# Kernel optimization log

Hardware: AMD Instinct MI355X
Metric: run time of the kernel (lower is better)

Reference implementation:

```python
import jax, jax.numpy as jnp
import numpy as np

B, N, NREL = 8, 512, 4096
IN_DIM, REL_DIM = 64, 32
NF_PART, NF_REL, NF_EFF, OUT_DIM = 128, 256, 128, 64


def _lin(key, fan_in, fan_out):
    kw, kb = jax.random.split(key)
    s = 1.0 / np.sqrt(fan_in)
    w = jax.random.uniform(kw, (fan_in, fan_out), jnp.float32, -s, s)
    b = jax.random.uniform(kb, (fan_out,), jnp.float32, -s, s)
    return w, b


def setup_inputs() -> dict:
    key = jax.random.key(0)
    ks = jax.random.split(key, 16)
    state = jax.random.normal(ks[0], (B, N, IN_DIM), jnp.float32)
    # one-hot receiver / sender incidence matrices [B, N, NREL]
    recv = jax.random.randint(ks[1], (B, NREL), 0, N)
    send = jax.random.randint(ks[2], (B, NREL), 0, N)
    Rr = jnp.transpose(jax.nn.one_hot(recv, N, dtype=jnp.float32), (0, 2, 1))
    Rs = jnp.transpose(jax.nn.one_hot(send, N, dtype=jnp.float32), (0, 2, 1))
    Ra = jax.random.normal(ks[3], (B, NREL, REL_DIM), jnp.float32)

    pe0_w, pe0_b = _lin(ks[4], IN_DIM, NF_PART)
    pe1_w, pe1_b = _lin(ks[5], NF_PART, NF_PART)
    pe2_w, pe2_b = _lin(ks[6], NF_PART, NF_EFF)
    re_in = 2 * IN_DIM + REL_DIM
    re0_w, re0_b = _lin(ks[7], re_in, NF_REL)
    re1_w, re1_b = _lin(ks[8], NF_REL, NF_REL)
    re2_w, re2_b = _lin(ks[9], NF_REL, NF_REL)
    rp_w, rp_b = _lin(ks[10], NF_REL + 2 * NF_EFF, NF_EFF)   # relation propagator
    pp_w, pp_b = _lin(ks[11], 2 * NF_EFF, NF_EFF)            # particle propagator
    pr0_w, pr0_b = _lin(ks[12], NF_EFF, NF_EFF)
    pr1_w, pr1_b = _lin(ks[13], NF_EFF, OUT_DIM)

    return dict(state=state, Rr=Rr, Rs=Rs, Ra=Ra,
                pe0_w=pe0_w, pe0_b=pe0_b, pe1_w=pe1_w, pe1_b=pe1_b,
                pe2_w=pe2_w, pe2_b=pe2_b,
                re0_w=re0_w, re0_b=re0_b, re1_w=re1_w, re1_b=re1_b,
                re2_w=re2_w, re2_b=re2_b,
                rp_w=rp_w, rp_b=rp_b, pp_w=pp_w, pp_b=pp_b,
                pr0_w=pr0_w, pr0_b=pr0_b, pr1_w=pr1_w, pr1_b=pr1_b,
                pstep=3)


def _mlp3(x, w0, b0, w1, b1, w2, b2):
    x = jax.nn.relu(x @ w0 + b0)
    x = jax.nn.relu(x @ w1 + b1)
    return jax.nn.relu(x @ w2 + b2)


def reference(state, Rr, Rs, Ra,
              pe0_w, pe0_b, pe1_w, pe1_b, pe2_w, pe2_b,
              re0_w, re0_b, re1_w, re1_b, re2_w, re2_b,
              rp_w, rp_b, pp_w, pp_b,
              pr0_w, pr0_b, pr1_w, pr1_b, pstep):
    Rrp = jnp.transpose(Rr, (0, 2, 1))  # [B, NREL, N]
    Rsp = jnp.transpose(Rs, (0, 2, 1))
    state_r = Rrp @ state               # [B, NREL, IN_DIM]
    state_s = Rsp @ state

    particle_encode = _mlp3(state, pe0_w, pe0_b, pe1_w, pe1_b, pe2_w, pe2_b)
    relation_encode = _mlp3(jnp.concatenate([state_r, state_s, Ra], axis=2),
                            re0_w, re0_b, re1_w, re1_b, re2_w, re2_b)

    particle_effect = jnp.zeros((state.shape[0], state.shape[1], NF_EFF),
                                dtype=state.dtype)
    for _ in range(pstep):
        effect_r = Rrp @ particle_effect           # gather to relations
        effect_s = Rsp @ particle_effect
        relation_effect = jax.nn.relu(
            jnp.concatenate([relation_encode, effect_r, effect_s], axis=2)
            @ rp_w + rp_b)
        effect_agg = Rr @ relation_effect          # scatter to particles
        particle_effect = jax.nn.relu(
            jnp.concatenate([particle_encode, effect_agg], axis=2)
            @ pp_w + pp_b)

    h = jax.nn.relu(particle_effect @ pr0_w + pr0_b)
    return h @ pr1_w + pr1_b                       # [B, N, OUT_DIM]
```

## Files before the change

### kernel.cpp

```cpp
#include <hip/hip_runtime.h>
#include <hip/hip_bf16.h>

#define BC    8
#define NC    512
#define NRELC 4096
#define MAXDEG 64

typedef unsigned short u16;
typedef __attribute__((ext_vector_type(2))) float  f32x2;
typedef __attribute__((ext_vector_type(4))) float  f32x4;
typedef __attribute__((ext_vector_type(8))) __bf16 bf16x8;
typedef __attribute__((ext_vector_type(8))) short  s16x8;
typedef __attribute__((ext_vector_type(2))) u16    u16x2;
typedef __attribute__((ext_vector_type(4))) u16    u16x4;
typedef __attribute__((ext_vector_type(4))) int    i32x4;

__device__ __forceinline__ u16 f2b(float f) {
  union { float f; unsigned u; } v; v.f = f;
  unsigned u = v.u;
  return (u16)((u + 0x7fffu + ((u >> 16) & 1u)) >> 16);
}
__device__ __forceinline__ float b2f(u16 h) {
  union { unsigned u; float f; } v; v.u = ((unsigned)h) << 16; return v.f;
}

template<int KBLK>
__device__ __forceinline__ int toff(int row, int k) {
  return (row >> 4) * (KBLK * 256) + ((k >> 3) << 8) + ((row & 15) << 4) + ((k & 7) << 1);
}

__global__ __launch_bounds__(1024, 8) void onehot_matvec_v2(
    const float* __restrict__ Rr, const float* __restrict__ Rs,
    int* __restrict__ recv, int* __restrict__ send) {
  int blk = blockIdx.x;
  int tens = blk >> 8;
  int b = (blk >> 5) & 7;
  int rt = blk & 31;
  const float* srcf = (tens ? Rs : Rr) + (long)b * NC * NRELC + rt * 128;
  int* dst = (tens ? send : recv) + b * NRELC + rt * 128;
  int tid = threadIdx.x;
  int ng = tid >> 5;
  int col = tid & 31;
  const f32x4* cp = (const f32x4*)srcf + col;
  f32x4 acc = (f32x4){0.f, 0.f, 0.f, 0.f};
#pragma unroll
  for (int i = 0; i < 16; ++i) {
    int n = ng * 16 + i;
    f32x4 x = cp[(long)n * (NRELC / 4)];
    float w = (float)n;
    acc[0] = fmaf(x[0], w, acc[0]);
    acc[1] = fmaf(x[1], w, acc[1]);
    acc[2] = fmaf(x[2], w, acc[2]);
    acc[3] = fmaf(x[3], w, acc[3]);
  }
  __shared__ f32x4 red[1024];
  red[tid] = acc;
  __syncthreads();
  if (tid < 32) {
    f32x4 s = red[tid];
#pragma unroll
    for (int g = 1; g < 32; ++g) {
      f32x4 t = red[g * 32 + tid];
      s[0] += t[0]; s[1] += t[1]; s[2] += t[2]; s[3] += t[3];
    }
    i32x4 o;
    o[0] = (int)s[0]; o[1] = (int)s[1]; o[2] = (int)s[2]; o[3] = (int)s[3];
    *(i32x4*)&dst[tid * 4] = o;
  }
}

struct WT13 {
  const float* src[13];
  u16* dst[13];
  int K[13], N[13];
  int cum[14];
};

__global__ void wtrans_v2(WT13 wt) {
  int idx = blockIdx.x * 256 + threadIdx.x;
  if (idx >= wt.cum[13]) return;
  int w = 0;
  while (idx >= wt.cum[w + 1]) ++w;
  int j = idx - wt.cum[w];
  int N = wt.N[w], K = wt.K[w];
  int k = j / N, n = j - k * N;
  wt.dst[w][n * K + k] = f2b(wt.src[w][j]);
}

template<int MT, int NT, bool AF32>
__device__ __forceinline__ void tile_gemm(const void* __restrict__ Ap, long rowBase,
                                          const u16* __restrict__ Wt, int n0,
                                          int K, int rl, int kg, f32x4 acc[MT][NT]) {
#pragma unroll
  for (int mt = 0; mt < MT; ++mt)
#pragma unroll
    for (int t = 0; t < NT; ++t) acc[mt][t] = (f32x4){0.f, 0.f, 0.f, 0.f};

  for (int k0 = 0; k0 < K; k0 += 32) {
    int kk = k0 + kg * 8;
    bf16x8 af[MT];
#pragma unroll
    for (int mt = 0; mt < MT; ++mt) {
      long row = rowBase + mt * 16 + rl;
      if (AF32) {
        const float* ap = (const float*)Ap + row * K + kk;
        f32x4 lo = *(const f32x4*)ap;
        f32x4 hi = *(const f32x4*)(ap + 4);
        s16x8 s;
        s[0] = (short)f2b(lo[0]); s[1] = (short)f2b(lo[1]);
        s[2] = (short)f2b(lo[2]); s[3] = (short)f2b(lo[3]);
        s[4] = (short)f2b(hi[0]); s[5] = (short)f2b(hi[1]);
        s[6] = (short)f2b(hi[2]); s[7] = (short)f2b(hi[3]);
        af[mt] = __builtin_bit_cast(bf16x8, s);
      } else {
        af[mt] = *reinterpret_cast<const bf16x8*>((const u16*)Ap + row * K + kk);
      }
    }
#pragma unroll
    for (int t = 0; t < NT; ++t) {
      bf16x8 bf = *reinterpret_cast<const bf16x8*>(Wt + (size_t)(n0 + t * 16 + rl) * K + kk);
#pragma unroll
      for (int mt = 0; mt < MT; ++mt)
        acc[mt][t] = __builtin_amdgcn_mfma_f32_16x16x32_bf16(af[mt], bf, acc[mt][t], 0, 0, 0);
    }
  }
}

__global__ __launch_bounds__(256) void csr_partenc_v2(
    const int* __restrict__ recv, int* __restrict__ deg, int* __restrict__ lists,
    const float* __restrict__ state,
    const u16* __restrict__ pe0t, const float* __restrict__ pe0_b,
    const u16* __restrict__ pe1t, const float* __restrict__ pe1_b,
    const u16* __restrict__ pe2t, const float* __restrict__ pe2_b,
    const u16* __restrict__ pp0t, const float* __restrict__ pp_b,
    float* __restrict__ pbase) {
  __shared__ char t0[4096];
  __shared__ char t1[4096];
  int wid = threadIdx.x >> 6, lane = threadIdx.x & 63;
  if (blockIdx.x < 1024) {
    int bn = blockIdx.x * 4 + wid;
    int b = bn >> 9, n = bn & 511;
    const int* rv = recv + (long)b * NRELC;
    int base = 0;
    for (int c = 0; c < 64; ++c) {
      int r = c * 64 + lane;
      bool ok = (rv[r] == n);
      unsigned long long m = __ballot(ok);
      if (ok) {
        int rank = __popcll(m & ((1ull << lane) - 1ull));
        lists[(long)bn * MAXDEG + base + rank] = r;
      }
      base += (int)__popcll(m);
    }
    if (lane == 0) deg[bn] = base;
    return;
  }
  int rl = lane & 15, kg = lane >> 4;
  long rowBase = (blockIdx.x - 1024) * 16;

  f32x4 acc[1][2];
  tile_gemm<1, 2, true>(state, rowBase, pe0t, wid * 32, 64, rl, kg, acc);
#pragma unroll
  for (int t = 0; t < 2; ++t) {
    int gc = wid * 32 + t * 16 + rl;
    float bv = pe0_b[gc];
#pragma unroll
    for (int r = 0; r < 4; ++r)
      *(u16*)&t0[toff<16>(kg * 4 + r, gc)] = f2b(fmaxf(acc[0][t][r] + bv, 0.f));
  }
  __syncthreads();

  f32x4 a2[2];
  a2[0] = (f32x4){0.f, 0.f, 0.f, 0.f};
  a2[1] = (f32x4){0.f, 0.f, 0.f, 0.f};
#pragma unroll
  for (int ki = 0; ki < 4; ++ki) {
    int kk = ki * 32 + kg * 8;
    bf16x8 af = *(const bf16x8*)&t0[toff<16>(rl, kk)];
#pragma unroll
    for (int t = 0; t < 2; ++t) {
      bf16x8 bf = *(const bf16x8*)(pe1t + (size_t)(wid * 32 + t * 16 + rl) * 128 + kk);
      a2[t] = __builtin_amdgcn_mfma_f32_16x16x32_bf16(af, bf, a2[t], 0, 0, 0);
    }
  }
#pragma unroll
  for (int t = 0; t < 2; ++t) {
    int gc = wid * 32 + t * 16 + rl;
    float bv = pe1_b[gc];
#pragma unroll
    for (int r = 0; r < 4; ++r)
      *(u16*)&t1[toff<16>(kg * 4 + r, gc)] = f2b(fmaxf(a2[t][r] + bv, 0.f));
  }
  __syncthreads();

  a2[0] = (f32x4){0.f, 0.f, 0.f, 0.f};
  a2[1] = (f32x4){0.f, 0.f, 0.f, 0.f};
#pragma unroll
  for (int ki = 0; ki < 4; ++ki) {
    int kk = ki * 32 + kg * 8;
    bf16x8 af = *(const bf16x8*)&t1[toff<16>(rl, kk)];
#pragma unroll
    for (int t = 0; t < 2; ++t) {
      bf16x8 bf = *(const bf16x8*)(pe2t + (size_t)(wid * 32 + t * 16 + rl) * 128 + kk);
      a2[t] = __builtin_amdgcn_mfma_f32_16x16x32_bf16(af, bf, a2[t], 0, 0, 0);
    }
  }
#pragma unroll
  for (int t = 0; t < 2; ++t) {
    int gc = wid * 32 + t * 16 + rl;
    float bv = pe2_b[gc];
#pragma unroll
    for (int r = 0; r < 4; ++r)
      *(u16*)&t0[toff<16>(kg * 4 + r, gc)] = f2b(fmaxf(a2[t][r] + bv, 0.f));
  }
  __syncthreads();

  a2[0] = (f32x4){0.f, 0.f, 0.f, 0.f};
  a2[1] = (f32x4){0.f, 0.f, 0.f, 0.f};
#pragma unroll
  for (int ki = 0; ki < 4; ++ki) {
    int kk = ki * 32 + kg * 8;
    bf16x8 af = *(const bf16x8*)&t0[toff<16>(rl, kk)];
#pragma unroll
    for (int t = 0; t < 2; ++t) {
      bf16x8 bf = *(const bf16x8*)(pp0t + (size_t)(wid * 32 + t * 16 + rl) * 128 + kk);
      a2[t] = __builtin_amdgcn_mfma_f32_16x16x32_bf16(af, bf, a2[t], 0, 0, 0);
    }
  }
#pragma unroll
  for (int t = 0; t < 2; ++t) {
    int gc = wid * 32 + t * 16 + rl;
    float bv = pp_b[gc];
#pragma unroll
    for (int r = 0; r < 4; ++r) {
      long gr = rowBase + kg * 4 + r;
      pbase[gr * 128 + gc] = a2[t][r] + bv;
    }
  }
}

template<int KD, int NTt>
__device__ __forceinline__ void lds_layer_v4(const char* bufIn, const u16* __restrict__ Wt,
                                             int n0, int rl, int kg, f32x4 acc[4][NTt]) {
  constexpr int KI = KD / 32;
  bf16x8 bw[NTt][KI];
#pragma unroll
  for (int t = 0; t < NTt; ++t)
#pragma unroll
    for (int ki = 0; ki < KI; ++ki)
      bw[t][ki] = *(const bf16x8*)(Wt + (size_t)(n0 + t * 16 + rl) * KD + ki * 32 + kg * 8);
#pragma unroll
  for (int mt = 0; mt < 4; ++mt)
#pragma unroll
    for (int t = 0; t < NTt; ++t) acc[mt][t] = (f32x4){0.f, 0.f, 0.f, 0.f};
#pragma unroll
  for (int ki = 0; ki < KI; ++ki) {
    int kk = ki * 32 + kg * 8;
    bf16x8 af[4];
#pragma unroll
    for (int mt = 0; mt < 4; ++mt)
      af[mt] = *(const bf16x8*)&bufIn[toff<32>(mt * 16 + rl, kk)];
#pragma unroll
    for (int t = 0; t < NTt; ++t)
#pragma unroll
      for (int mt = 0; mt < 4; ++mt)
        acc[mt][t] = __builtin_amdgcn_mfma_f32_16x16x32_bf16(af[mt], bw[t][ki], acc[mt][t], 0, 0, 0);
  }
}

template<int NTt>
__device__ __forceinline__ void lds_store_v4(char* bufOut, const float* __restrict__ bias,
                                             int n0, int rl, int kg, f32x4 acc[4][NTt]) {
#pragma unroll
  for (int mt = 0; mt < 4; ++mt)
#pragma unroll
    for (int t = 0; t < NTt; ++t) {
      int gc = n0 + t * 16 + rl;
      float bv = bias[gc];
#pragma unroll
      for (int r = 0; r < 4; ++r) {
        int row = mt * 16 + kg * 4 + r;
        *(u16*)&bufOut[toff<32>(row, gc)] = f2b(fmaxf(acc[mt][t][r] + bv, 0.f));
      }
    }
}

__global__ __launch_bounds__(512, 3) void relenc_fused_v5(
    const float* __restrict__ state, const float* __restrict__ Ra,
    const int* __restrict__ recv, const int* __restrict__ send,
    const u16* __restrict__ re0t, const float* __restrict__ re0_b,
    const u16* __restrict__ re1t, const float* __restrict__ re1_b,
    const u16* __restrict__ re2t, const float* __restrict__ re2_b,
    const u16* __restrict__ rp0t, const float* __restrict__ rp_b,
    u16* __restrict__ rbase16) {
  __shared__ char bufA[32768];
  __shared__ char bufB[32768];
  int tid = threadIdx.x;
  int m0 = blockIdx.x * 64;

  for (int c = tid; c < 64 * 40; c += 512) {
    int row = c / 40;
    int c4 = (c - row * 40) * 4;
    int grow = m0 + row;
    int b = grow >> 12;
    f32x4 v;
    if (c4 < 64)       v = *(const f32x4*)&state[((long)(b * NC + recv[grow])) * 64 + c4];
    else if (c4 < 128) v = *(const f32x4*)&state[((long)(b * NC + send[grow])) * 64 + (c4 - 64)];
    else               v = *(const f32x4*)&Ra[(long)grow * 32 + (c4 - 128)];
    u16x4 o;
    o[0] = f2b(v[0]); o[1] = f2b(v[1]); o[2] = f2b(v[2]); o[3] = f2b(v[3]);
    *(u16x4*)&bufA[toff<32>(row, c4)] = o;
  }
  __syncthreads();

  int wid = tid >> 6, lane = tid & 63;
  int rl = lane & 15, kg = lane >> 4;

  f32x4 acc[4][2];
  lds_layer_v4<160, 2>(bufA, re0t, wid * 32, rl, kg, acc);
  lds_store_v4<2>(bufB, re0_b, wid * 32, rl, kg, acc);
  __syncthreads();
  lds_layer_v4<256, 2>(bufB, re1t, wid * 32, rl, kg, acc);
  lds_store_v4<2>(bufA, re1_b, wid * 32, rl, kg, acc);
  __syncthreads();
  lds_layer_v4<256, 2>(bufA, re2t, wid * 32, rl, kg, acc);
  lds_store_v4<2>(bufB, re2_b, wid * 32, rl, kg, acc);
  __syncthreads();
  f32x4 acc2[4][1];
  lds_layer_v4<256, 1>(bufB, rp0t, wid * 16, rl, kg, acc2);
#pragma unroll
  for (int mt = 0; mt < 4; ++mt) {
    int gc = wid * 16 + rl;
    float bv = rp_b[gc];
#pragma unroll
    for (int r = 0; r < 4; ++r) {
      long gr = m0 + mt * 16 + kg * 4 + r;
      rbase16[gr * 128 + gc] = f2b(acc2[mt][0][r] + bv);
    }
  }
}

__global__ __launch_bounds__(512, 4) void relstep_v5(
    const u16* __restrict__ peff, const u16* __restrict__ rp1t,
    const u16* __restrict__ rp2t, const u16* __restrict__ rbase16,
    const int* __restrict__ recv, const int* __restrict__ send,
    u16* __restrict__ tmp16) {
  __shared__ char ebuf0[16384];
  __shared__ char ebuf1[16384];
  int tid = threadIdx.x;
  int m0 = blockIdx.x * 64;

  for (int c = tid; c < 2048; c += 512) {
    int s = c >> 10, rem = c & 1023, row = rem >> 4, ch = rem & 15;
    int gr = m0 + row;
    int b = gr >> 12;
    int idx = s ? send[gr] : recv[gr];
    bf16x8 v = *(const bf16x8*)&peff[((long)(b * NC + idx)) * 128 + ch * 8];
    char* dst = s ? ebuf1 : ebuf0;
    *(bf16x8*)&dst[toff<16>(row, ch * 8)] = v;
  }
  __syncthreads();

  int wid = tid >> 6, lane = tid & 63;
  int rl = lane & 15, kg = lane >> 4;
  int wm = wid >> 2, wn = wid & 3;
  int n0 = wn * 32;

  bf16x8 b1[2][4], b2[2][4];
#pragma unroll
  for (int t = 0; t < 2; ++t)
#pragma unroll
    for (int ki = 0; ki < 4; ++ki) {
      b1[t][ki] = *(const bf16x8*)(rp1t + (size_t)(n0 + t * 16 + rl) * 128 + ki * 32 + kg * 8);
      b2[t][ki] = *(const bf16x8*)(rp2t + (size_t)(n0 + t * 16 + rl) * 128 + ki * 32 + kg * 8);
    }

  f32x4 acc[2][2];
#pragma unroll
  for (int mt = 0; mt < 2; ++mt)
#pragma unroll
    for (int t = 0; t < 2; ++t) acc[mt][t] = (f32x4){0.f, 0.f, 0.f, 0.f};

#pragma unroll
  for (int ki = 0; ki < 4; ++ki) {
    int kk = ki * 32 + kg * 8;
    bf16x8 e0[2], e1[2];
#pragma unroll
    for (int mt = 0; mt < 2; ++mt) {
      int row = wm * 32 + mt * 16 + rl;
      e0[mt] = *(const bf16x8*)&ebuf0[toff<16>(row, kk)];
      e1[mt] = *(const bf16x8*)&ebuf1[toff<16>(row, kk)];
    }
#pragma unroll
    for (int t = 0; t < 2; ++t)
#pragma unroll
      for (int mt = 0; mt < 2; ++mt)
        acc[mt][t] = __builtin_amdgcn_mfma_f32_16x16x32_bf16(e0[mt], b1[t][ki], acc[mt][t], 0, 0, 0);
#pragma unroll
    for (int t = 0; t < 2; ++t)
#pragma unroll
      for (int mt = 0; mt < 2; ++mt)
        acc[mt][t] = __builtin_amdgcn_mfma_f32_16x16x32_bf16(e1[mt], b2[t][ki], acc[mt][t], 0, 0, 0);
  }

#pragma unroll
  for (int mt = 0; mt < 2; ++mt) {
#pragma unroll
    for (int r = 0; r < 4; ++r) {
      long gr = m0 + wm * 32 + mt * 16 + kg * 4 + r;
      const u16* rb = &rbase16[gr * 128];
      u16* dst = &tmp16[gr * 128];
#pragma unroll
      for (int t = 0; t < 2; ++t) {
        int gc = n0 + t * 16 + rl;
        dst[gc] = f2b(fmaxf(acc[mt][t][r] + b2f(rb[gc]), 0.f));
      }
    }
  }
}

template<bool RELU>
__global__ __launch_bounds__(256) void segreduce_b16(
    const u16* __restrict__ src, const int* __restrict__ deg,
    const int* __restrict__ lists, u16* __restrict__ agg16) {
  int wid = threadIdx.x >> 6, lane = threadIdx.x & 63;
  int p = blockIdx.x * 4 + wid;
  int b = p >> 9;
  int c = lane * 2;
  int d = deg[p];
  const int* lp = &lists[(long)p * MAXDEG];
  f32x2 acc = (f32x2){0.f, 0.f};
  for (int k = 0; k < d; ++k) {
    long row = ((long)b * NRELC + lp[k]) * 128;
    u16x2 h = *(const u16x2*)&src[row + c];
    float v0 = b2f(h[0]), v1 = b2f(h[1]);
    if (RELU) { v0 = fmaxf(v0, 0.f); v1 = fmaxf(v1, 0.f); }
    acc[0] += v0; acc[1] += v1;
  }
  u16x2 o;
  o[0] = f2b(acc[0]); o[1] = f2b(acc[1]);
  *(u16x2*)&agg16[(long)p * 128 + c] = o;
}

__global__ __launch_bounds__(256) void ppgemm_v2(
    const u16* __restrict__ agg16, const u16* __restrict__ pp1t,
    const float* __restrict__ pbase, u16* __restrict__ peff) {
  int wid = threadIdx.x >> 6, lane = threadIdx.x & 63;
  int rl = lane & 15, kg = lane >> 4;
  long rowBase = blockIdx.x * 16;
  f32x4 acc[1][2];
  tile_gemm<1, 2, false>(agg16, rowBase, pp1t, wid * 32, 128, rl, kg, acc);
#pragma unroll
  for (int t = 0; t < 2; ++t) {
    int gc = wid * 32 + t * 16 + rl;
#pragma unroll
    for (int r = 0; r < 4; ++r) {
      long gr = rowBase + kg * 4 + r;
      float v = acc[0][t][r] + pbase[gr * 128 + gc];
      peff[gr * 128 + gc] = f2b(fmaxf(v, 0.f));
    }
  }
}

__global__ __launch_bounds__(256) void ppdec_kernel(
    const u16* __restrict__ agg16, const u16* __restrict__ pp1t,
    const float* __restrict__ pbase,
    const u16* __restrict__ pr0t, const float* __restrict__ pr0_b,
    const u16* __restrict__ pr1t, const float* __restrict__ pr1_b,
    float* __restrict__ out) {
  __shared__ char t0[4096];
  __shared__ char t1[4096];
  int wid = threadIdx.x >> 6, lane = threadIdx.x & 63;
  int rl = lane & 15, kg = lane >> 4;
  long rowBase = blockIdx.x * 16;

  f32x4 acc[1][2];
  tile_gemm<1, 2, false>(agg16, rowBase, pp1t, wid * 32, 128, rl, kg, acc);
#pragma unroll
  for (int t = 0; t < 2; ++t) {
    int gc = wid * 32 + t * 16 + rl;
#pragma unroll
    for (int r = 0; r < 4; ++r) {
      int row = kg * 4 + r;
      float v = acc[0][t][r] + pbase[(rowBase + row) * 128 + gc];
      *(u16*)&t0[toff<16>(row, gc)] = f2b(fmaxf(v, 0.f));
    }
  }
  __syncthreads();

  f32x4 a2[2];
  a2[0] = (f32x4){0.f, 0.f, 0.f, 0.f};
  a2[1] = (f32x4){0.f, 0.f, 0.f, 0.f};
#pragma unroll
  for (int ki = 0; ki < 4; ++ki) {
    int kk = ki * 32 + kg * 8;
    bf16x8 af = *(const bf16x8*)&t0[toff<16>(rl, kk)];
#pragma unroll
    for (int t = 0; t < 2; ++t) {
      bf16x8 bf = *(const bf16x8*)(pr0t + (size_t)(wid * 32 + t * 16 + rl) * 128 + kk);
      a2[t] = __builtin_amdgcn_mfma_f32_16x16x32_bf16(af, bf, a2[t], 0, 0, 0);
    }
  }
#pragma unroll
  for (int t = 0; t < 2; ++t) {
    int gc = wid * 32 + t * 16 + rl;
    float bv = pr0_b[gc];
#pragma unroll
    for (int r = 0; r < 4; ++r) {
      int row = kg * 4 + r;
      *(u16*)&t1[toff<16>(row, gc)] = f2b(fmaxf(a2[t][r] + bv, 0.f));
    }
  }
  __syncthreads();

  if (wid < 4) {
    f32x4 a3 = (f32x4){0.f, 0.f, 0.f, 0.f};
#pragma unroll
    for (int ki = 0; ki < 4; ++ki) {
      int kk = ki * 32 + kg * 8;
      bf16x8 af = *(const bf16x8*)&t1[toff<16>(rl, kk)];
      bf16x8 bf = *(const bf16x8*)(pr1t + (size_t)(wid * 16 + rl) * 128 + kk);
      a3 = __builtin_amdgcn_mfma_f32_16x16x32_bf16(af, bf, a3, 0, 0, 0);
    }
    int gc = wid * 16 + rl;
    float bv = pr1_b[gc];
#pragma unroll
    for (int r = 0; r < 4; ++r) {
      long gr = rowBase + kg * 4 + r;
      out[gr * 64 + gc] = a3[r] + bv;
    }
  }
}

extern "C" void kernel_launch(void* const* d_in, const int* in_sizes, int n_in,
                              void* d_out, int out_size, void* d_ws, size_t ws_size,
                              hipStream_t stream) {
  const float* state = (const float*)d_in[0];
  const float* Rr    = (const float*)d_in[1];
  const float* Rs    = (const float*)d_in[2];
  const float* Ra    = (const float*)d_in[3];
  const float* pe0_w = (const float*)d_in[4];  const float* pe0_b = (const float*)d_in[5];
  const float* pe1_w = (const float*)d_in[6];  const float* pe1_b = (const float*)d_in[7];
  const float* pe2_w = (const float*)d_in[8];  const float* pe2_b = (const float*)d_in[9];
  const float* re0_w = (const float*)d_in[10]; const float* re0_b = (const float*)d_in[11];
  const float* re1_w = (const float*)d_in[12]; const float* re1_b = (const float*)d_in[13];
  const float* re2_w = (const float*)d_in[14]; const float* re2_b = (const float*)d_in[15];
  const float* rp_w  = (const float*)d_in[16]; const float* rp_b  = (const float*)d_in[17];
  const float* pp_w  = (const float*)d_in[18]; const float* pp_b  = (const float*)d_in[19];
  const float* pr0_w = (const float*)d_in[20]; const float* pr0_b = (const float*)d_in[21];
  const float* pr1_w = (const float*)d_in[22]; const float* pr1_b = (const float*)d_in[23];

  char* base = (char*)d_ws; size_t off = 0;
  auto alloc = [&](size_t b) -> void* {
    void* p = base + off; off = (off + b + 255) & ~(size_t)255; return p;
  };

  int* recv  = (int*)alloc(4L * BC * NRELC);
  int* send  = (int*)alloc(4L * BC * NRELC);
  int* deg   = (int*)alloc(4L * BC * NC);
  int* lists = (int*)alloc(4L * BC * NC * MAXDEG);
  u16* pe0t = (u16*)alloc(2L * 128 * 64);
  u16* pe1t = (u16*)alloc(2L * 128 * 128);
  u16* pe2t = (u16*)alloc(2L * 128 * 128);
  u16* re0t = (u16*)alloc(2L * 256 * 160);
  u16* re1t = (u16*)alloc(2L * 256 * 256);
  u16* re2t = (u16*)alloc(2L * 256 * 256);
  u16* rp0t = (u16*)alloc(2L * 128 * 256);
  u16* rp1t = (u16*)alloc(2L * 128 * 128);
  u16* rp2t = (u16*)alloc(2L * 128 * 128);
  u16* pp0t = (u16*)alloc(2L * 128 * 128);
  u16* pp1t = (u16*)alloc(2L * 128 * 128);
  u16* pr0t = (u16*)alloc(2L * 128 * 128);
  u16* pr1t = (u16*)alloc(2L * 64 * 128);
  u16* tmp16   = (u16*)alloc(2L * 32768 * 128);
  u16* rbase16 = (u16*)alloc(2L * 32768 * 128);
  float* pbase = (float*)alloc(4L * 4096 * 128);
  u16* agg16 = (u16*)alloc(2L * 4096 * 128);
  u16* peff = (u16*)alloc(2L * 4096 * 128);
  (void)ws_size; (void)in_sizes; (void)n_in; (void)out_size;

  struct WSpec { const float* src; u16* dst; int K, N; };
  const WSpec specs[13] = {
      {pe0_w,            pe0t, 64, 128},
      {pe1_w,            pe1t, 128, 128},
      {pe2_w,            pe2t, 128, 128},
      {re0_w,            re0t, 160, 256},
      {re1_w,            re1t, 256, 256},
      {re2_w,            re2t, 256, 256},
      {rp_w,             rp0t, 256, 128},
      {rp_w + 256 * 128, rp1t, 128, 128},
      {rp_w + 384 * 128, rp2t, 128, 128},
      {pp_w,             pp0t, 128, 128},
      {pp_w + 128 * 128, pp1t, 128, 128},
      {pr0_w,            pr0t, 128, 128},
      {pr1_w,            pr1t, 128, 64},
  };
  WT13 wt;
  int cum = 0;
  for (int i = 0; i < 13; ++i) {
    wt.src[i] = specs[i].src; wt.dst[i] = specs[i].dst;
    wt.K[i] = specs[i].K; wt.N[i] = specs[i].N;
    wt.cum[i] = cum; cum += specs[i].K * specs[i].N;
  }
  wt.cum[13] = cum;

  onehot_matvec_v2<<<512, 1024, 0, stream>>>(Rr, Rs, recv, send);
  wtrans_v2<<<(cum + 255) / 256, 256, 0, stream>>>(wt);

  csr_partenc_v2<<<1280, 256, 0, stream>>>(recv, deg, lists, state,
                                           pe0t, pe0_b, pe1t, pe1_b, pe2t, pe2_b,
                                           pp0t, pp_b, pbase);
  relenc_fused_v5<<<512, 512, 0, stream>>>(state, Ra, recv, send,
                                           re0t, re0_b, re1t, re1_b, re2t, re2_b,
                                           rp0t, rp_b, rbase16);

  segreduce_b16<true><<<1024, 256, 0, stream>>>(rbase16, deg, lists, agg16);
  ppgemm_v2<<<256, 256, 0, stream>>>(agg16, pp1t, pbase, peff);
  for (int s = 1; s < 3; ++s) {
    relstep_v5<<<512, 512, 0, stream>>>(peff, rp1t, rp2t, rbase16, recv, send, tmp16);
    segreduce_b16<false><<<1024, 256, 0, stream>>>(tmp16, deg, lists, agg16);
    if (s == 2) break;
    ppgemm_v2<<<256, 256, 0, stream>>>(agg16, pp1t, pbase, peff);
  }

  ppdec_kernel<<<256, 256, 0, stream>>>(agg16, pp1t, pbase,
                                        pr0t, pr0_b, pr1t, pr1_b, (float*)d_out);
}
```

Baseline: 159.2 us.

## Fuse segment reduction with particle-propagator GEMM and decoder into one kernel

Merges the per-particle segment-sum over incident relations with the following particle-propagator GEMM, and in the last step also with the two decoder layers, into one 1024-thread kernel. Each block reduces 16 particles (one per wave) into shared memory, then four waves run the MFMA GEMM directly from LDS. This drops the agg16 intermediate buffer and three kernel launches. In exchange, 12 of the 16 waves sit idle during the GEMM phase and each block is large.

```diff
diff --git a/kernel.cpp b/kernel.cpp
--- a/kernel.cpp
+++ b/kernel.cpp
@@ -419,106 +419,120 @@
   }
 }
 
-template<bool RELU>
-__global__ __launch_bounds__(256) void segreduce_b16(
+template<bool SRELU, bool FINAL>
+__global__ __launch_bounds__(1024) void segpp_v3(
     const u16* __restrict__ src, const int* __restrict__ deg,
-    const int* __restrict__ lists, u16* __restrict__ agg16) {
-  int wid = threadIdx.x >> 6, lane = threadIdx.x & 63;
-  int p = blockIdx.x * 4 + wid;
-  int b = p >> 9;
-  int c = lane * 2;
-  int d = deg[p];
-  const int* lp = &lists[(long)p * MAXDEG];
-  f32x2 acc = (f32x2){0.f, 0.f};
-  for (int k = 0; k < d; ++k) {
-    long row = ((long)b * NRELC + lp[k]) * 128;
-    u16x2 h = *(const u16x2*)&src[row + c];
-    float v0 = b2f(h[0]), v1 = b2f(h[1]);
-    if (RELU) { v0 = fmaxf(v0, 0.f); v1 = fmaxf(v1, 0.f); }
-    acc[0] += v0; acc[1] += v1;
-  }
-  u16x2 o;
-  o[0] = f2b(acc[0]); o[1] = f2b(acc[1]);
-  *(u16x2*)&agg16[(long)p * 128 + c] = o;
-}
-
-__global__ __launch_bounds__(256) void ppgemm_v2(
-    const u16* __restrict__ agg16, const u16* __restrict__ pp1t,
-    const float* __restrict__ pbase, u16* __restrict__ peff) {
-  int wid = threadIdx.x >> 6, lane = threadIdx.x & 63;
-  int rl = lane & 15, kg = lane >> 4;
-  long rowBase = blockIdx.x * 16;
-  f32x4 acc[1][2];
-  tile_gemm<1, 2, false>(agg16, rowBase, pp1t, wid * 32, 128, rl, kg, acc);
-#pragma unroll
-  for (int t = 0; t < 2; ++t) {
-    int gc = wid * 32 + t * 16 + rl;
-#pragma unroll
-    for (int r = 0; r < 4; ++r) {
-      long gr = rowBase + kg * 4 + r;
-      float v = acc[0][t][r] + pbase[gr * 128 + gc];
-      peff[gr * 128 + gc] = f2b(fmaxf(v, 0.f));
-    }
-  }
-}
-
-__global__ __launch_bounds__(256) void ppdec_kernel(
-    const u16* __restrict__ agg16, const u16* __restrict__ pp1t,
-    const float* __restrict__ pbase,
+    const int* __restrict__ lists, const u16* __restrict__ pp1t,
+    const float* __restrict__ pbase, u16* __restrict__ peff,
     const u16* __restrict__ pr0t, const float* __restrict__ pr0_b,
     const u16* __restrict__ pr1t, const float* __restrict__ pr1_b,
     float* __restrict__ out) {
   __shared__ char t0[4096];
   __shared__ char t1[4096];
-  int wid = threadIdx.x >> 6, lane = threadIdx.x & 63;
+  int tid = threadIdx.x, wid = tid >> 6, lane = tid & 63;
+  long p0 = (long)blockIdx.x * 16;
+
+  {
+    int p = (int)p0 + wid;
+    int b = p >> 9;
+    int c = lane * 2;
+    int d = deg[p];
+    const int* lp = &lists[(long)p * MAXDEG];
+    f32x2 a = (f32x2){0.f, 0.f};
+    for (int k = 0; k < d; ++k) {
+      long row = ((long)b * NRELC + lp[k]) * 128;
+      u16x2 h = *(const u16x2*)&src[row + c];
+      float v0 = b2f(h[0]), v1 = b2f(h[1]);
+      if (SRELU) { v0 = fmaxf(v0, 0.f); v1 = fmaxf(v1, 0.f); }
+      a[0] += v0; a[1] += v1;
+    }
+    u16x2 o;
+    o[0] = f2b(a[0]); o[1] = f2b(a[1]);
+    *(u16x2*)&t0[toff<16>(wid, c)] = o;
+  }
+  __syncthreads();
+
   int rl = lane & 15, kg = lane >> 4;
-  long rowBase = blockIdx.x * 16;
-
-  f32x4 acc[1][2];
-  tile_gemm<1, 2, false>(agg16, rowBase, pp1t, wid * 32, 128, rl, kg, acc);
-#pragma unroll
-  for (int t = 0; t < 2; ++t) {
-    int gc = wid * 32 + t * 16 + rl;
-#pragma unroll
-    for (int r = 0; r < 4; ++r) {
-      int row = kg * 4 + r;
-      float v = acc[0][t][r] + pbase[(rowBase + row) * 128 + gc];
-      *(u16*)&t0[toff<16>(row, gc)] = f2b(fmaxf(v, 0.f));
-    }
-  }
-  __syncthreads();
-
-  f32x4 a2[2];
-  a2[0] = (f32x4){0.f, 0.f, 0.f, 0.f};
-  a2[1] = (f32x4){0.f, 0.f, 0.f, 0.f};
-#pragma unroll
-  for (int ki = 0; ki < 4; ++ki) {
-    int kk = ki * 32 + kg * 8;
-    bf16x8 af = *(const bf16x8*)&t0[toff<16>(rl, kk)];
+
+  f32x4 pa[2];
+  pa[0] = (f32x4){0.f, 0.f, 0.f, 0.f};
+  pa[1] = (f32x4){0.f, 0.f, 0.f, 0.f};
+  if (wid < 4) {
+#pragma unroll
+    for (int ki = 0; ki < 4; ++ki) {
+      int kk = ki * 32 + kg * 8;
+      bf16x8 af = *(const bf16x8*)&t0[toff<16>(rl, kk)];
+#pragma unroll
+      for (int t = 0; t < 2; ++t) {
+        bf16x8 bf = *(const bf16x8*)(pp1t + (size_t)(wid * 32 + t * 16 + rl) * 128 + kk);
+        pa[t] = __builtin_amdgcn_mfma_f32_16x16x32_bf16(af, bf, pa[t], 0, 0, 0);
+      }
+    }
+  }
+
+  if (!FINAL) {
+    if (wid < 4) {
+#pragma unroll
+      for (int t = 0; t < 2; ++t) {
+        int gc = wid * 32 + t * 16 + rl;
+#pragma unroll
+        for (int r = 0; r < 4; ++r) {
+          long gr = p0 + kg * 4 + r;
+          float v = pa[t][r] + pbase[gr * 128 + gc];
+          peff[gr * 128 + gc] = f2b(fmaxf(v, 0.f));
+        }
+      }
+    }
+    return;
+  }
+
+  if (wid < 4) {
 #pragma unroll
     for (int t = 0; t < 2; ++t) {
-      bf16x8 bf = *(const bf16x8*)(pr0t + (size_t)(wid * 32 + t * 16 + rl) * 128 + kk);
-      a2[t] = __builtin_amdgcn_mfma_f32_16x16x32_bf16(af, bf, a2[t], 0, 0, 0);
-    }
-  }
-#pragma unroll
-  for (int t = 0; t < 2; ++t) {
-    int gc = wid * 32 + t * 16 + rl;
-    float bv = pr0_b[gc];
-#pragma unroll
-    for (int r = 0; r < 4; ++r) {
-      int row = kg * 4 + r;
-      *(u16*)&t1[toff<16>(row, gc)] = f2b(fmaxf(a2[t][r] + bv, 0.f));
-    }
-  }
-  __syncthreads();
-
+      int gc = wid * 32 + t * 16 + rl;
+#pragma unroll
+      for (int r = 0; r < 4; ++r) {
+        int row = kg * 4 + r;
+        float v = pa[t][r] + pbase[(p0 + row) * 128 + gc];
+        *(u16*)&t1[toff<16>(row, gc)] = f2b(fmaxf(v, 0.f));
+      }
+    }
+  }
+  __syncthreads();
+
+  f32x4 ha[2];
+  ha[0] = (f32x4){0.f, 0.f, 0.f, 0.f};
+  ha[1] = (f32x4){0.f, 0.f, 0.f, 0.f};
   if (wid < 4) {
-    f32x4 a3 = (f32x4){0.f, 0.f, 0.f, 0.f};
 #pragma unroll
     for (int ki = 0; ki < 4; ++ki) {
       int kk = ki * 32 + kg * 8;
       bf16x8 af = *(const bf16x8*)&t1[toff<16>(rl, kk)];
+#pragma unroll
+      for (int t = 0; t < 2; ++t) {
+        bf16x8 bf = *(const bf16x8*)(pr0t + (size_t)(wid * 32 + t * 16 + rl) * 128 + kk);
+        ha[t] = __builtin_amdgcn_mfma_f32_16x16x32_bf16(af, bf, ha[t], 0, 0, 0);
+      }
+    }
+#pragma unroll
+    for (int t = 0; t < 2; ++t) {
+      int gc = wid * 32 + t * 16 + rl;
+      float bv = pr0_b[gc];
+#pragma unroll
+      for (int r = 0; r < 4; ++r) {
+        int row = kg * 4 + r;
+        *(u16*)&t0[toff<16>(row, gc)] = f2b(fmaxf(ha[t][r] + bv, 0.f));
+      }
+    }
+  }
+  __syncthreads();
+
+  if (wid < 4) {
+    f32x4 a3 = (f32x4){0.f, 0.f, 0.f, 0.f};
+#pragma unroll
+    for (int ki = 0; ki < 4; ++ki) {
+      int kk = ki * 32 + kg * 8;
+      bf16x8 af = *(const bf16x8*)&t0[toff<16>(rl, kk)];
       bf16x8 bf = *(const bf16x8*)(pr1t + (size_t)(wid * 16 + rl) * 128 + kk);
       a3 = __builtin_amdgcn_mfma_f32_16x16x32_bf16(af, bf, a3, 0, 0, 0);
     }
@@ -526,7 +540,7 @@
     float bv = pr1_b[gc];
 #pragma unroll
     for (int r = 0; r < 4; ++r) {
-      long gr = rowBase + kg * 4 + r;
+      long gr = p0 + kg * 4 + r;
       out[gr * 64 + gc] = a3[r] + bv;
     }
   }
@@ -575,7 +589,6 @@
   u16* tmp16   = (u16*)alloc(2L * 32768 * 128);
   u16* rbase16 = (u16*)alloc(2L * 32768 * 128);
   float* pbase = (float*)alloc(4L * 4096 * 128);
-  u16* agg16 = (u16*)alloc(2L * 4096 * 128);
   u16* peff = (u16*)alloc(2L * 4096 * 128);
   (void)ws_size; (void)in_sizes; (void)n_in; (void)out_size;
 
@@ -614,15 +627,15 @@
                                            re0t, re0_b, re1t, re1_b, re2t, re2_b,
                                            rp0t, rp_b, rbase16);
 
-  segreduce_b16<true><<<1024, 256, 0, stream>>>(rbase16, deg, lists, agg16);
-  ppgemm_v2<<<256, 256, 0, stream>>>(agg16, pp1t, pbase, peff);
-  for (int s = 1; s < 3; ++s) {
-    relstep_v5<<<512, 512, 0, stream>>>(peff, rp1t, rp2t, rbase16, recv, send, tmp16);
-    segreduce_b16<false><<<1024, 256, 0, stream>>>(tmp16, deg, lists, agg16);
-    if (s == 2) break;
-    ppgemm_v2<<<256, 256, 0, stream>>>(agg16, pp1t, pbase, peff);
-  }
-
-  ppdec_kernel<<<256, 256, 0, stream>>>(agg16, pp1t, pbase,
-                                        pr0t, pr0_b, pr1t, pr1_b, (float*)d_out);
-}
+  segpp_v3<true, false><<<256, 1024, 0, stream>>>(rbase16, deg, lists, pp1t,
+                                                  pbase, peff, pr0t, pr0_b,
+                                                  pr1t, pr1_b, nullptr);
+  relstep_v5<<<512, 512, 0, stream>>>(peff, rp1t, rp2t, rbase16, recv, send, tmp16);
+  segpp_v3<false, false><<<256, 1024, 0, stream>>>(tmp16, deg, lists, pp1t,
+                                                   pbase, peff, pr0t, pr0_b,
+                                                   pr1t, pr1_b, nullptr);
+  relstep_v5<<<512, 512, 0, stream>>>(peff, rp1t, rp2t, rbase16, recv, send, tmp16);
+  segpp_v3<false, true><<<256, 1024, 0, stream>>>(tmp16, deg, lists, pp1t,
+                                                  pbase, nullptr, pr0t, pr0_b,
+                                                  pr1t, pr1_b, (float*)d_out);
+}
```

After: 144.0 us. 1.11x faster.
